# Kernel tuning notes

Hardware: AMD Instinct MI355X
Metric: run time of the kernel (lower is better)

Reference implementation:

```python
import jax, jax.numpy as jnp
import numpy as np

D_MODEL = 64

def setup_inputs() -> dict:
    key = jax.random.key(0)
    k1, k2, k3, k4 = jax.random.split(key, 4)
    B, T, E = 4, 4096, 128
    x = jax.random.normal(k1, (B, T, E), dtype=jnp.float32)
    # nn.Linear weights, stored transposed as (in, out) for x @ W
    s = 1.0 / np.sqrt(E)
    Wq = jax.random.uniform(k2, (E, D_MODEL), jnp.float32, -s, s)
    Wk = jax.random.uniform(k3, (E, D_MODEL), jnp.float32, -s, s)
    Wv = jax.random.uniform(k4, (E, D_MODEL), jnp.float32, -s, s)
    return {"x": x, "Wq": Wq, "Wk": Wk, "Wv": Wv}

def reference(x, Wq, Wk, Wv):
    B, T, E = x.shape
    q = jnp.einsum('bte,ed->btd', x, Wq)
    k = jnp.einsum('bte,ed->btd', x, Wk)
    v = jnp.einsum('bte,ed->btd', x, Wv)
    scores = jnp.einsum('bqd,bkd->bqk', q, k) / np.sqrt(D_MODEL)  # [B,T,T]
    causal = jnp.tril(jnp.ones((T, T), dtype=bool))
    scores = jnp.where(causal, scores, jnp.float32(-1e9))
    attn = jax.nn.softmax(scores, axis=-1)
    # dropout p=0.0 -> identity (eval-mode faithful)
    return jnp.einsum('bqk,bkd->bqd', attn, v)
```

## Files before the change

### kernel.cpp

```cpp
#include <hip/hip_runtime.h>
#include <hip/hip_bf16.h>


typedef __attribute__((ext_vector_type(4))) float  f32x4;
typedef __attribute__((ext_vector_type(4))) unsigned int u32x4;
typedef __attribute__((ext_vector_type(8))) __bf16 bf16x8;
typedef __attribute__((ext_vector_type(8))) unsigned short u16x8;
typedef __attribute__((ext_vector_type(4))) unsigned short u16x4;

#define T_SEQ 4096
#define DH    64
#define EDIM  128
#define KVB   64
#define QSCALE 0.18033688f
#define NTRI  528

__device__ __forceinline__ unsigned short f2bf(float f) {
    unsigned int x = __builtin_bit_cast(unsigned int, f);
    unsigned int r = x + 0x7fffu + ((x >> 16) & 1u);
    return (unsigned short)(r >> 16);
}

__device__ __forceinline__ unsigned int cvt_pk_bf16(float lo, float hi) {
    unsigned int d;
    asm("v_cvt_pk_bf16_f32 %0, %1, %2" : "=v"(d) : "v"(lo), "v"(hi));
    return d;
}

__device__ __forceinline__ f32x4 mfma_bf16(u16x8 a, u16x8 b, f32x4 c) {
    return __builtin_amdgcn_mfma_f32_16x16x32_bf16(
        __builtin_bit_cast(bf16x8, a), __builtin_bit_cast(bf16x8, b), c, 0, 0, 0);
}

__device__ __forceinline__ int kswz(int row, int bcol) {
    return row * 128 + (bcol ^ ((row & 7) << 4));
}
__device__ __forceinline__ int vswz(int row, int bcol) {
    return row * 256 + (bcol ^ ((row & 15) << 4));
}

__global__ __launch_bounds__(256) void prep_w_kernel(
    const float* __restrict__ wq, const float* __restrict__ wk,
    const float* __restrict__ wv, unsigned short* __restrict__ wt)
{
    int o = blockIdx.x * 256 + threadIdx.x;
    int m   = o >> 13;
    int rem = o & 8191;
    int d = rem >> 7, e = rem & 127;
    const float* W = (m == 0) ? wq : (m == 1) ? wk : wv;
    wt[o] = f2bf(W[e * DH + d]);
}

__global__ __launch_bounds__(64) void proj_kernel(
    const float* __restrict__ x, const unsigned short* __restrict__ wt,
    unsigned short* __restrict__ qw, unsigned short* __restrict__ kw,
    unsigned short* __restrict__ vt)
{
    const int l   = threadIdx.x;
    const int l15 = l & 15;
    const int lg  = l >> 4;
    const int row0 = blockIdx.x * 16;
    const int b    = row0 >> 12;
    const int t0   = row0 & 4095;

    u16x8 af[4];
    #pragma unroll
    for (int kt = 0; kt < 4; ++kt) {
        const float* xp = x + (row0 + l15) * EDIM + kt * 32 + lg * 8;
        f32x4 a = *(const f32x4*)xp;
        f32x4 bb = *(const f32x4*)(xp + 4);
        af[kt] = u16x8{ f2bf(a[0]), f2bf(a[1]), f2bf(a[2]), f2bf(a[3]),
                        f2bf(bb[0]), f2bf(bb[1]), f2bf(bb[2]), f2bf(bb[3]) };
    }

    unsigned short* outs[2] = { qw, kw };
    #pragma unroll
    for (int m = 0; m < 2; ++m) {
        #pragma unroll
        for (int nt = 0; nt < 4; ++nt) {
            f32x4 acc = {};
            #pragma unroll
            for (int kt = 0; kt < 4; ++kt) {
                u16x8 bfrag = *(const u16x8*)(wt + (m * 64 + nt * 16 + l15) * EDIM
                                                 + kt * 32 + lg * 8);
                acc = mfma_bf16(af[kt], bfrag, acc);
            }
            const float sc = (m == 0) ? QSCALE : 1.0f;
            #pragma unroll
            for (int r = 0; r < 4; ++r)
                outs[m][(row0 + lg * 4 + r) * DH + nt * 16 + l15] = f2bf(acc[r] * sc);
        }
    }

    #pragma unroll
    for (int nt = 0; nt < 4; ++nt) {
        f32x4 acc = {};
        #pragma unroll
        for (int kt = 0; kt < 4; ++kt) {
            u16x8 bfrag = *(const u16x8*)(wt + (2 * 64 + nt * 16 + l15) * EDIM
                                             + kt * 32 + lg * 8);
            acc = mfma_bf16(af[kt], bfrag, acc);
        }
        u16x4 pv = { f2bf(acc[0]), f2bf(acc[1]), f2bf(acc[2]), f2bf(acc[3]) };
        *(u16x4*)(vt + ((size_t)(b * DH + nt * 16 + l15)) * T_SEQ + t0 + lg * 4) = pv;
    }
}

__global__ __launch_bounds__(256, 4) void attn_partial_kernel(
    const unsigned short* __restrict__ qg, const unsigned short* __restrict__ kg,
    const unsigned short* __restrict__ vt,
    unsigned short* __restrict__ po, float* __restrict__ pm, float* __restrict__ pl)
{
    const int bid = blockIdx.x;
    const int b   = bid / NTRI;
    const int i   = bid - b * NTRI;
    int q = (int)((__builtin_sqrtf((float)(8 * i + 1)) - 1.0f) * 0.5f);
    while (q * (q + 1) / 2 > i) --q;
    while ((q + 1) * (q + 2) / 2 <= i) ++q;
    const int q128 = q;
    const int ch   = i - q * (q + 1) / 2;

    __shared__ char K_ldsb[128 * 128];
    __shared__ char V_ldsb[64 * 256];

    const int tid = threadIdx.x;
    const int w   = tid >> 6;
    const int l   = tid & 63;
    const int l15 = l & 15;
    const int lg  = l >> 4;

    const int base   = b * T_SEQ;
    const int qrow0w = q128 * 128 + w * 32;
    const int kvb    = ch * 128;

    const unsigned short* kgB = kg + (size_t)base * DH;
    const unsigned short* vtB = vt + (size_t)b * DH * T_SEQ;

    {
        u16x8 kr[4], vr[4];
        #pragma unroll
        for (int j = 0; j < 4; ++j) {
            int gi = tid + j * 256;
            kr[j] = *(const u16x8*)(kgB + (size_t)(kvb + (gi >> 3)) * DH + (gi & 7) * 8);
            vr[j] = *(const u16x8*)(vtB + (size_t)(gi >> 4) * T_SEQ + kvb + (gi & 15) * 8);
        }
        #pragma unroll
        for (int j = 0; j < 4; ++j) {
            int gi = tid + j * 256;
            *(u16x8*)&K_ldsb[kswz(gi >> 3, (gi & 7) * 16)]  = kr[j];
            *(u16x8*)&V_ldsb[vswz(gi >> 4, (gi & 15) * 16)] = vr[j];
        }
    }

    u16x8 qf[2][2];
    #pragma unroll
    for (int rt = 0; rt < 2; ++rt) {
        const unsigned short* qrow = qg + (base + qrow0w + rt * 16 + l15) * DH;
        qf[rt][0] = *(const u16x8*)(qrow + 0 + lg * 8);
        qf[rt][1] = *(const u16x8*)(qrow + 32 + lg * 8);
    }

    f32x4 o_acc[2][4];
    float m_run[2], l_run[2];
    #pragma unroll
    for (int rt = 0; rt < 2; ++rt) {
        #pragma unroll
        for (int dt = 0; dt < 4; ++dt) o_acc[rt][dt] = f32x4{};
        m_run[rt] = -1e30f; l_run[rt] = 0.0f;
    }

    const int src0 = l15 + 32 * (lg & 1);
    const int src1 = src0 + 16;
    const bool hi  = (lg >> 1) != 0;

    __syncthreads();

    #pragma unroll
    for (int tt = 0; tt < 2; ++tt) {
        const int kv0 = kvb + tt * 64;
        if (kv0 > qrow0w + 31) continue;

        u16x8 kf[4][2];
        #pragma unroll
        for (int nt = 0; nt < 4; ++nt)
            #pragma unroll
            for (int kt = 0; kt < 2; ++kt) {
                int krow = tt * 64 + nt * 16 + l15;
                kf[nt][kt] = *(const u16x8*)&K_ldsb[kswz(krow, kt * 64 + lg * 16)];
            }

        f32x4 s[2][4];
        __builtin_amdgcn_s_setprio(1);
        #pragma unroll
        for (int rt = 0; rt < 2; ++rt)
            #pragma unroll
            for (int nt = 0; nt < 4; ++nt) {
                f32x4 a = {};
                a = mfma_bf16(kf[nt][0], qf[rt][0], a);
                a = mfma_bf16(kf[nt][1], qf[rt][1], a);
                s[rt][nt] = a;
            }
        __builtin_amdgcn_s_setprio(0);

        if (kv0 + KVB - 1 > qrow0w) {
            #pragma unroll
            for (int rt = 0; rt < 2; ++rt)
                #pragma unroll
                for (int nt = 0; nt < 4; ++nt)
                    #pragma unroll
                    for (int rr = 0; rr < 4; ++rr) {
                        int kj = kv0 + nt * 16 + lg * 4 + rr;
                        int qi = qrow0w + rt * 16 + l15;
                        if (kj > qi) s[rt][nt][rr] = -1e30f;
                    }
        }

        float sc2[2];
        bool grow = false;
        unsigned int pk[2][4][2];
        #pragma unroll
        for (int rt = 0; rt < 2; ++rt) {
            float mx = s[rt][0][0];
            #pragma unroll
            for (int nt = 0; nt < 4; ++nt)
                #pragma unroll
                for (int rr = 0; rr < 4; ++rr)
                    mx = fmaxf(mx, s[rt][nt][rr]);
            mx = fmaxf(mx, __shfl_xor(mx, 16));
            mx = fmaxf(mx, __shfl_xor(mx, 32));

            float mold = m_run[rt];
            float mnew = fmaxf(mold, mx);
            grow |= (mx > mold);
            float sc = exp2f(mold - mnew);
            sc2[rt] = sc;
            m_run[rt] = mnew;

            float rs = 0.0f;
            #pragma unroll
            for (int nt = 0; nt < 4; ++nt)
                #pragma unroll
                for (int rr = 0; rr < 4; ++rr) {
                    float p = exp2f(s[rt][nt][rr] - mnew);
                    s[rt][nt][rr] = p;
                    rs += p;
                }
            rs += __shfl_xor(rs, 16);
            rs += __shfl_xor(rs, 32);
            l_run[rt] = l_run[rt] * sc + rs;

            #pragma unroll
            for (int nt = 0; nt < 4; ++nt) {
                pk[rt][nt][0] = cvt_pk_bf16(s[rt][nt][0], s[rt][nt][1]);
                pk[rt][nt][1] = cvt_pk_bf16(s[rt][nt][2], s[rt][nt][3]);
            }
        }
        if (__any(grow)) {
            #pragma unroll
            for (int rt = 0; rt < 2; ++rt)
                #pragma unroll
                for (int dt = 0; dt < 4; ++dt)
                    o_acc[rt][dt] *= sc2[rt];
        }

        __builtin_amdgcn_s_setprio(1);
        #pragma unroll
        for (int kt = 0; kt < 2; ++kt) {
            u16x8 vf[4];
            #pragma unroll
            for (int dt = 0; dt < 4; ++dt) {
                int vrow = dt * 16 + l15;
                vf[dt] = *(const u16x8*)&V_ldsb[vswz(vrow, tt * 128 + kt * 64 + lg * 16)];
            }
            #pragma unroll
            for (int rt = 0; rt < 2; ++rt) {
                unsigned int pb[4];
                #pragma unroll
                for (int t = 0; t < 4; ++t) {
                    int src = (t < 2) ? src0 : src1;
                    unsigned int pa  = __shfl(pk[rt][2 * kt][t & 1], src);
                    unsigned int pbv = __shfl(pk[rt][2 * kt + 1][t & 1], src);
                    pb[t] = hi ? pbv : pa;
                }
                u32x4 pbq = { pb[0], pb[1], pb[2], pb[3] };
                u16x8 pbf = __builtin_bit_cast(u16x8, pbq);
                #pragma unroll
                for (int dt = 0; dt < 4; ++dt)
                    o_acc[rt][dt] = mfma_bf16(vf[dt], pbf, o_acc[rt][dt]);
            }
        }
        __builtin_amdgcn_s_setprio(0);
    }

    const int pidx = bid;
    unsigned short* pob = po + (size_t)pidx * 8192;
    #pragma unroll
    for (int rt = 0; rt < 2; ++rt) {
        int row = w * 32 + rt * 16 + l15;
        #pragma unroll
        for (int dt = 0; dt < 4; ++dt) {
            unsigned int w0 = cvt_pk_bf16(o_acc[rt][dt][0], o_acc[rt][dt][1]);
            unsigned int w1 = cvt_pk_bf16(o_acc[rt][dt][2], o_acc[rt][dt][3]);
            *(unsigned int*)&pob[row * 64 + dt * 16 + lg * 4]     = w0;
            *(unsigned int*)&pob[row * 64 + dt * 16 + lg * 4 + 2] = w1;
        }
        if (lg == 0) {
            pm[pidx * 128 + row] = m_run[rt];
            pl[pidx * 128 + row] = l_run[rt];
        }
    }
}

__global__ __launch_bounds__(256) void attn_combine_kernel(
    const unsigned short* __restrict__ po, const float* __restrict__ pm,
    const float* __restrict__ pl, float* __restrict__ out)
{
    const int blk   = blockIdx.x;
    const int slice = blk & 3;
    const int tb    = blk >> 2;
    const int q128  = tb & 31;
    const int b     = tb >> 5;
    const int nch   = q128 + 1;
    const int bslot = b * NTRI + q128 * (q128 + 1) / 2;
    const int row   = slice * 32 + (threadIdx.x >> 3);
    const int d0    = (threadIdx.x & 7) * 8;

    float m_i[32];
    #pragma unroll
    for (int i = 0; i < 32; ++i) {
        int ii = (i < nch) ? i : 0;
        m_i[i] = pm[(bslot + ii) * 128 + row];
    }
    float mstar = m_i[0];
    #pragma unroll
    for (int i = 1; i < 32; ++i)
        if (i < nch) mstar = fmaxf(mstar, m_i[i]);

    float lsum = 0.0f;
    float a[8] = {};
    #pragma unroll
    for (int i = 0; i < 32; ++i) {
        if (i < nch) {
            float wi = exp2f(m_i[i] - mstar);
            lsum += wi * pl[(bslot + i) * 128 + row];
            u16x8 v = *(const u16x8*)&po[(size_t)(bslot + i) * 8192 + row * 64 + d0];
            #pragma unroll
            for (int j = 0; j < 8; ++j) {
                unsigned int u = (unsigned int)v[j] << 16;
                a[j] += wi * __builtin_bit_cast(float, u);
            }
        }
    }
    const float inv = 1.0f / lsum;
    float* op = out + (size_t)(b * T_SEQ + q128 * 128 + row) * DH + d0;
    f32x4 o0 = { a[0] * inv, a[1] * inv, a[2] * inv, a[3] * inv };
    f32x4 o1 = { a[4] * inv, a[5] * inv, a[6] * inv, a[7] * inv };
    *(f32x4*)op = o0;
    *(f32x4*)(op + 4) = o1;
}

__global__ __launch_bounds__(64, 4) void attn_direct_kernel(
    const unsigned short* __restrict__ qg, const unsigned short* __restrict__ kg,
    const unsigned short* __restrict__ vt, float* __restrict__ out)
{
    const int bid = blockIdx.x;
    const int q32 = bid & 127;
    const int b   = bid >> 7;
    const int l = threadIdx.x, l15 = l & 15, lg = l >> 4;
    const int qrow0 = q32 * 32;
    const int base  = b * T_SEQ;
    const unsigned short* kp = kg + (size_t)base * DH;
    const unsigned short* vp = vt + (size_t)b * DH * T_SEQ;

    u16x8 qf[2][2];
    #pragma unroll
    for (int rt = 0; rt < 2; ++rt) {
        const unsigned short* qrow = qg + (base + qrow0 + rt * 16 + l15) * DH;
        qf[rt][0] = *(const u16x8*)(qrow + 0 + lg * 8);
        qf[rt][1] = *(const u16x8*)(qrow + 32 + lg * 8);
    }

    f32x4 o_acc[2][4];
    float m_run[2], l_run[2];
    #pragma unroll
    for (int rt = 0; rt < 2; ++rt) {
        #pragma unroll
        for (int dt = 0; dt < 4; ++dt) o_acc[rt][dt] = f32x4{};
        m_run[rt] = -1e30f; l_run[rt] = 0.0f;
    }

    const int src0 = l15 + 32 * (lg & 1);
    const int src1 = src0 + 16;
    const bool hi  = (lg >> 1) != 0;

    for (int kv0 = 0; kv0 <= qrow0 + 31; kv0 += KVB) {
        u16x8 kf[4][2];
        #pragma unroll
        for (int nt = 0; nt < 4; ++nt)
            #pragma unroll
            for (int kt = 0; kt < 2; ++kt)
                kf[nt][kt] = *(const u16x8*)(kp + (kv0 + nt * 16 + l15) * DH
                                                + kt * 32 + lg * 8);
        f32x4 s[2][4];
        #pragma unroll
        for (int rt = 0; rt < 2; ++rt)
            #pragma unroll
            for (int nt = 0; nt < 4; ++nt) {
                f32x4 a = {};
                a = mfma_bf16(kf[nt][0], qf[rt][0], a);
                a = mfma_bf16(kf[nt][1], qf[rt][1], a);
                s[rt][nt] = a;
            }
        if (kv0 + KVB - 1 > qrow0) {
            #pragma unroll
            for (int rt = 0; rt < 2; ++rt)
                #pragma unroll
                for (int nt = 0; nt < 4; ++nt)
                    #pragma unroll
                    for (int rr = 0; rr < 4; ++rr) {
                        int kj = kv0 + nt * 16 + lg * 4 + rr;
                        int qi = qrow0 + rt * 16 + l15;
                        if (kj > qi) s[rt][nt][rr] = -1e30f;
                    }
        }
        float sc2[2];
        bool grow = false;
        unsigned int pk[2][4][2];
        #pragma unroll
        for (int rt = 0; rt < 2; ++rt) {
            float mx = s[rt][0][0];
            #pragma unroll
            for (int nt = 0; nt < 4; ++nt)
                #pragma unroll
                for (int rr = 0; rr < 4; ++rr)
                    mx = fmaxf(mx, s[rt][nt][rr]);
            mx = fmaxf(mx, __shfl_xor(mx, 16));
            mx = fmaxf(mx, __shfl_xor(mx, 32));
            float mold = m_run[rt];
            float mnew = fmaxf(mold, mx);
            grow |= (mx > mold);
            float sc = exp2f(mold - mnew);
            sc2[rt] = sc;
            m_run[rt] = mnew;
            float rs = 0.0f;
            #pragma unroll
            for (int nt = 0; nt < 4; ++nt)
                #pragma unroll
                for (int rr = 0; rr < 4; ++rr) {
                    float p = exp2f(s[rt][nt][rr] - mnew);
                    s[rt][nt][rr] = p;
                    rs += p;
                }
            rs += __shfl_xor(rs, 16);
            rs += __shfl_xor(rs, 32);
            l_run[rt] = l_run[rt] * sc + rs;
            #pragma unroll
            for (int nt = 0; nt < 4; ++nt) {
                pk[rt][nt][0] = cvt_pk_bf16(s[rt][nt][0], s[rt][nt][1]);
                pk[rt][nt][1] = cvt_pk_bf16(s[rt][nt][2], s[rt][nt][3]);
            }
        }
        if (__any(grow)) {
            #pragma unroll
            for (int rt = 0; rt < 2; ++rt)
                #pragma unroll
                for (int dt = 0; dt < 4; ++dt)
                    o_acc[rt][dt] *= sc2[rt];
        }
        #pragma unroll
        for (int kt = 0; kt < 2; ++kt) {
            u16x8 vf[4];
            #pragma unroll
            for (int dt = 0; dt < 4; ++dt)
                vf[dt] = *(const u16x8*)(vp + (size_t)(dt * 16 + l15) * T_SEQ
                                            + kv0 + kt * 32 + lg * 8);
            #pragma unroll
            for (int rt = 0; rt < 2; ++rt) {
                unsigned int pb[4];
                #pragma unroll
                for (int t = 0; t < 4; ++t) {
                    int src = (t < 2) ? src0 : src1;
                    unsigned int pa  = __shfl(pk[rt][2 * kt][t & 1], src);
                    unsigned int pbv = __shfl(pk[rt][2 * kt + 1][t & 1], src);
                    pb[t] = hi ? pbv : pa;
                }
                u32x4 pbq = { pb[0], pb[1], pb[2], pb[3] };
                u16x8 pbf = __builtin_bit_cast(u16x8, pbq);
                #pragma unroll
                for (int dt = 0; dt < 4; ++dt)
                    o_acc[rt][dt] = mfma_bf16(vf[dt], pbf, o_acc[rt][dt]);
            }
        }
    }

    #pragma unroll
    for (int rt = 0; rt < 2; ++rt) {
        float inv = 1.0f / l_run[rt];
        int row = base + qrow0 + rt * 16 + l15;
        #pragma unroll
        for (int dt = 0; dt < 4; ++dt) {
            f32x4 ov = o_acc[rt][dt] * inv;
            *(f32x4*)&out[(size_t)row * DH + dt * 16 + lg * 4] = ov;
        }
    }
}

extern "C" void kernel_launch(void* const* d_in, const int* in_sizes, int n_in,
                              void* d_out, int out_size, void* d_ws, size_t ws_size,
                              hipStream_t stream)
{
    const float* x  = (const float*)d_in[0];
    const float* wq = (const float*)d_in[1];
    const float* wk = (const float*)d_in[2];
    const float* wv = (const float*)d_in[3];
    float* out = (float*)d_out;

    unsigned short* wt = (unsigned short*)d_ws;
    unsigned short* qw = (unsigned short*)((char*)d_ws + 65536);
    unsigned short* kw = qw + (size_t)16384 * DH;
    unsigned short* vt = kw + (size_t)16384 * DH;

    const size_t slots  = 4u * NTRI;
    const size_t po_off = 65536u + 3u * 16384u * DH * 2u;
    const size_t po_sz  = slots * 8192 * 2;
    const size_t pm_off = po_off + po_sz;
    const size_t pl_off = pm_off + slots * 128 * 4;
    const size_t need   = pl_off + slots * 128 * 4;

    prep_w_kernel<<<96, 256, 0, stream>>>(wq, wk, wv, wt);
    proj_kernel<<<1024, 64, 0, stream>>>(x, wt, qw, kw, vt);

    if (ws_size >= need) {
        unsigned short* po = (unsigned short*)((char*)d_ws + po_off);
        float* pm = (float*)((char*)d_ws + pm_off);
        float* pl = (float*)((char*)d_ws + pl_off);
        attn_partial_kernel<<<4 * NTRI, 256, 0, stream>>>(qw, kw, vt, po, pm, pl);
        attn_combine_kernel<<<4 * 32 * 4, 256, 0, stream>>>(po, pm, pl, out);
    } else {
        attn_direct_kernel<<<4 * 128, 64, 0, stream>>>(qw, kw, vt, out);
    }
}
```

Baseline: 60.02 us.

## Process two KV chunks per attention block with register prefetch

Each partial-attention block now covers up to 256 keys instead of 128, which cuts the number of blocks from 528 to 272 per batch and halves the partial outputs the combine kernel reads. The second 128-key chunk is loaded into registers while the first is computed, then written to LDS between barriers. The row-sum shuffles are moved out of the inner loop to a single reduction at the end, and the max and sum reductions use a tree order. The trade-offs are fewer blocks to fill the GPU, longer serial work per block, and extra barriers.

```diff
diff --git a/kernel.cpp b/kernel.cpp
--- a/kernel.cpp
+++ b/kernel.cpp
@@ -13,7 +13,7 @@
 #define EDIM  128
 #define KVB   64
 #define QSCALE 0.18033688f
-#define NTRI  528
+#define NPAIR 272
 
 __device__ __forceinline__ unsigned short f2bf(float f) {
     unsigned int x = __builtin_bit_cast(unsigned int, f);
@@ -106,19 +106,42 @@
     }
 }
 
+__device__ __forceinline__ void loadKV(u16x8 kr[4], u16x8 vr[4],
+                                       const unsigned short* kgB,
+                                       const unsigned short* vtB,
+                                       int kv0, int tid) {
+    #pragma unroll
+    for (int j = 0; j < 4; ++j) {
+        int gi = tid + j * 256;
+        kr[j] = *(const u16x8*)(kgB + (size_t)(kv0 + (gi >> 3)) * DH + (gi & 7) * 8);
+        vr[j] = *(const u16x8*)(vtB + (size_t)(gi >> 4) * T_SEQ + kv0 + (gi & 15) * 8);
+    }
+}
+__device__ __forceinline__ void writeKV(const u16x8 kr[4], const u16x8 vr[4],
+                                        char* K_ldsb, char* V_ldsb, int tid) {
+    #pragma unroll
+    for (int j = 0; j < 4; ++j) {
+        int gi = tid + j * 256;
+        *(u16x8*)&K_ldsb[kswz(gi >> 3, (gi & 7) * 16)]  = kr[j];
+        *(u16x8*)&V_ldsb[vswz(gi >> 4, (gi & 15) * 16)] = vr[j];
+    }
+}
+
 __global__ __launch_bounds__(256, 4) void attn_partial_kernel(
     const unsigned short* __restrict__ qg, const unsigned short* __restrict__ kg,
     const unsigned short* __restrict__ vt,
     unsigned short* __restrict__ po, float* __restrict__ pm, float* __restrict__ pl)
 {
     const int bid = blockIdx.x;
-    const int b   = bid / NTRI;
-    const int i   = bid - b * NTRI;
-    int q = (int)((__builtin_sqrtf((float)(8 * i + 1)) - 1.0f) * 0.5f);
-    while (q * (q + 1) / 2 > i) --q;
-    while ((q + 1) * (q + 2) / 2 <= i) ++q;
-    const int q128 = q;
-    const int ch   = i - q * (q + 1) / 2;
+    const int b   = bid / NPAIR;
+    const int i   = bid - b * NPAIR;
+    int k = (int)((__builtin_sqrtf((float)(4 * i + 1)) - 1.0f) * 0.5f);
+    while (k * (k + 1) > i) --k;
+    while ((k + 1) * (k + 2) <= i) ++k;
+    const int r    = i - k * (k + 1);
+    const int hiq  = (r >= k + 1);
+    const int q128 = 2 * k + hiq;
+    const int ch   = hiq ? r - (k + 1) : r;
 
     __shared__ char K_ldsb[128 * 128];
     __shared__ char V_ldsb[64 * 256];
@@ -131,26 +154,12 @@
 
     const int base   = b * T_SEQ;
     const int qrow0w = q128 * 128 + w * 32;
-    const int kvb    = ch * 128;
+    const int kvb    = ch * 256;
+    const int kve    = min(kvb + 256, q128 * 128 + 128);
+    const bool ng2   = (kve - kvb) > 128;
 
     const unsigned short* kgB = kg + (size_t)base * DH;
     const unsigned short* vtB = vt + (size_t)b * DH * T_SEQ;
-
-    {
-        u16x8 kr[4], vr[4];
-        #pragma unroll
-        for (int j = 0; j < 4; ++j) {
-            int gi = tid + j * 256;
-            kr[j] = *(const u16x8*)(kgB + (size_t)(kvb + (gi >> 3)) * DH + (gi & 7) * 8);
-            vr[j] = *(const u16x8*)(vtB + (size_t)(gi >> 4) * T_SEQ + kvb + (gi & 15) * 8);
-        }
-        #pragma unroll
-        for (int j = 0; j < 4; ++j) {
-            int gi = tid + j * 256;
-            *(u16x8*)&K_ldsb[kswz(gi >> 3, (gi & 7) * 16)]  = kr[j];
-            *(u16x8*)&V_ldsb[vswz(gi >> 4, (gi & 15) * 16)] = vr[j];
-        }
-    }
 
     u16x8 qf[2][2];
     #pragma unroll
@@ -173,12 +182,8 @@
     const int src1 = src0 + 16;
     const bool hi  = (lg >> 1) != 0;
 
-    __syncthreads();
-
-    #pragma unroll
-    for (int tt = 0; tt < 2; ++tt) {
-        const int kv0 = kvb + tt * 64;
-        if (kv0 > qrow0w + 31) continue;
+    auto compute_tile = [&](int kv0, int tt) {
+        if (kv0 > qrow0w + 31) return;
 
         u16x8 kf[4][2];
         #pragma unroll
@@ -220,12 +225,15 @@
         unsigned int pk[2][4][2];
         #pragma unroll
         for (int rt = 0; rt < 2; ++rt) {
-            float mx = s[rt][0][0];
-            #pragma unroll
-            for (int nt = 0; nt < 4; ++nt)
-                #pragma unroll
-                for (int rr = 0; rr < 4; ++rr)
-                    mx = fmaxf(mx, s[rt][nt][rr]);
+            float t0 = fmaxf(fmaxf(s[rt][0][0], s[rt][0][1]),
+                             fmaxf(s[rt][0][2], s[rt][0][3]));
+            float t1 = fmaxf(fmaxf(s[rt][1][0], s[rt][1][1]),
+                             fmaxf(s[rt][1][2], s[rt][1][3]));
+            float t2 = fmaxf(fmaxf(s[rt][2][0], s[rt][2][1]),
+                             fmaxf(s[rt][2][2], s[rt][2][3]));
+            float t3 = fmaxf(fmaxf(s[rt][3][0], s[rt][3][1]),
+                             fmaxf(s[rt][3][2], s[rt][3][3]));
+            float mx = fmaxf(fmaxf(t0, t1), fmaxf(t2, t3));
             mx = fmaxf(mx, __shfl_xor(mx, 16));
             mx = fmaxf(mx, __shfl_xor(mx, 32));
 
@@ -236,23 +244,22 @@
             sc2[rt] = sc;
             m_run[rt] = mnew;
 
-            float rs = 0.0f;
+            float e[4][4];
             #pragma unroll
             for (int nt = 0; nt < 4; ++nt)
                 #pragma unroll
-                for (int rr = 0; rr < 4; ++rr) {
-                    float p = exp2f(s[rt][nt][rr] - mnew);
-                    s[rt][nt][rr] = p;
-                    rs += p;
-                }
-            rs += __shfl_xor(rs, 16);
-            rs += __shfl_xor(rs, 32);
-            l_run[rt] = l_run[rt] * sc + rs;
+                for (int rr = 0; rr < 4; ++rr)
+                    e[nt][rr] = exp2f(s[rt][nt][rr] - mnew);
+            float s0 = (e[0][0] + e[0][1]) + (e[0][2] + e[0][3]);
+            float s1 = (e[1][0] + e[1][1]) + (e[1][2] + e[1][3]);
+            float s2 = (e[2][0] + e[2][1]) + (e[2][2] + e[2][3]);
+            float s3 = (e[3][0] + e[3][1]) + (e[3][2] + e[3][3]);
+            l_run[rt] = l_run[rt] * sc + ((s0 + s1) + (s2 + s3));
 
             #pragma unroll
             for (int nt = 0; nt < 4; ++nt) {
-                pk[rt][nt][0] = cvt_pk_bf16(s[rt][nt][0], s[rt][nt][1]);
-                pk[rt][nt][1] = cvt_pk_bf16(s[rt][nt][2], s[rt][nt][3]);
+                pk[rt][nt][0] = cvt_pk_bf16(e[nt][0], e[nt][1]);
+                pk[rt][nt][1] = cvt_pk_bf16(e[nt][2], e[nt][3]);
             }
         }
         if (__any(grow)) {
@@ -290,12 +297,32 @@
             }
         }
         __builtin_amdgcn_s_setprio(0);
+    };
+
+    u16x8 kr[4], vr[4];
+    loadKV(kr, vr, kgB, vtB, kvb, tid);
+    writeKV(kr, vr, K_ldsb, V_ldsb, tid);
+    __syncthreads();
+
+    if (ng2) loadKV(kr, vr, kgB, vtB, kvb + 128, tid);
+    compute_tile(kvb, 0);
+    compute_tile(kvb + 64, 1);
+
+    if (ng2) {
+        __syncthreads();
+        writeKV(kr, vr, K_ldsb, V_ldsb, tid);
+        __syncthreads();
+        compute_tile(kvb + 128, 0);
+        compute_tile(kvb + 192, 1);
     }
 
     const int pidx = bid;
     unsigned short* pob = po + (size_t)pidx * 8192;
     #pragma unroll
     for (int rt = 0; rt < 2; ++rt) {
+        float lt = l_run[rt];
+        lt += __shfl_xor(lt, 16);
+        lt += __shfl_xor(lt, 32);
         int row = w * 32 + rt * 16 + l15;
         #pragma unroll
         for (int dt = 0; dt < 4; ++dt) {
@@ -306,7 +333,7 @@
         }
         if (lg == 0) {
             pm[pidx * 128 + row] = m_run[rt];
-            pl[pidx * 128 + row] = l_run[rt];
+            pl[pidx * 128 + row] = lt;
         }
     }
 }
@@ -320,26 +347,27 @@
     const int tb    = blk >> 2;
     const int q128  = tb & 31;
     const int b     = tb >> 5;
-    const int nch   = q128 + 1;
-    const int bslot = b * NTRI + q128 * (q128 + 1) / 2;
+    const int kk    = q128 >> 1;
+    const int nch   = kk + 1;
+    const int bslot = b * NPAIR + kk * (kk + 1) + (q128 & 1) * (kk + 1);
     const int row   = slice * 32 + (threadIdx.x >> 3);
     const int d0    = (threadIdx.x & 7) * 8;
 
-    float m_i[32];
-    #pragma unroll
-    for (int i = 0; i < 32; ++i) {
+    float m_i[16];
+    #pragma unroll
+    for (int i = 0; i < 16; ++i) {
         int ii = (i < nch) ? i : 0;
         m_i[i] = pm[(bslot + ii) * 128 + row];
     }
     float mstar = m_i[0];
     #pragma unroll
-    for (int i = 1; i < 32; ++i)
+    for (int i = 1; i < 16; ++i)
         if (i < nch) mstar = fmaxf(mstar, m_i[i]);
 
     float lsum = 0.0f;
     float a[8] = {};
     #pragma unroll
-    for (int i = 0; i < 32; ++i) {
+    for (int i = 0; i < 16; ++i) {
         if (i < nch) {
             float wi = exp2f(m_i[i] - mstar);
             lsum += wi * pl[(bslot + i) * 128 + row];
@@ -520,7 +548,7 @@
     unsigned short* kw = qw + (size_t)16384 * DH;
     unsigned short* vt = kw + (size_t)16384 * DH;
 
-    const size_t slots  = 4u * NTRI;
+    const size_t slots  = 4u * NPAIR;
     const size_t po_off = 65536u + 3u * 16384u * DH * 2u;
     const size_t po_sz  = slots * 8192 * 2;
     const size_t pm_off = po_off + po_sz;
@@ -534,7 +562,7 @@
         unsigned short* po = (unsigned short*)((char*)d_ws + po_off);
         float* pm = (float*)((char*)d_ws + pm_off);
         float* pl = (float*)((char*)d_ws + pl_off);
-        attn_partial_kernel<<<4 * NTRI, 256, 0, stream>>>(qw, kw, vt, po, pm, pl);
+        attn_partial_kernel<<<4 * NPAIR, 256, 0, stream>>>(qw, kw, vt, po, pm, pl);
         attn_combine_kernel<<<4 * 32 * 4, 256, 0, stream>>>(po, pm, pl, out);
     } else {
         attn_direct_kernel<<<4 * 128, 64, 0, stream>>>(qw, kw, vt, out);
```

After: 65.92 us. 9.8% more time.

## Widen split-KV attention blocks to 256 query rows with XCD-aware block mapping

Applied to the files above, without the earlier changes.

Each partial-attention block now handles 256 query rows (8 waves, 512 threads) against one 128-key chunk, so each K/V chunk loaded into LDS is reused by twice as many queries and the block count roughly halves. Block indices are remapped so that consecutive tiles are spread across the 8 XCDs. The triangular index decoding, the partial buffer strides and the combine kernel's slot indexing are updated to match. The cost is more chunks on the diagonal where half the rows are fully masked, which adds wasted work, plus higher register and occupancy pressure at 512 threads per block.

```diff
diff --git a/kernel.cpp b/kernel.cpp
--- a/kernel.cpp
+++ b/kernel.cpp
@@ -13,7 +13,7 @@
 #define EDIM  128
 #define KVB   64
 #define QSCALE 0.18033688f
-#define NTRI  528
+#define NTRI2 272
 
 __device__ __forceinline__ unsigned short f2bf(float f) {
     unsigned int x = __builtin_bit_cast(unsigned int, f);
@@ -106,19 +106,19 @@
     }
 }
 
-__global__ __launch_bounds__(256, 4) void attn_partial_kernel(
+__global__ __launch_bounds__(512, 6) void attn_partial_kernel(
     const unsigned short* __restrict__ qg, const unsigned short* __restrict__ kg,
     const unsigned short* __restrict__ vt,
     unsigned short* __restrict__ po, float* __restrict__ pm, float* __restrict__ pl)
 {
-    const int bid = blockIdx.x;
-    const int b   = bid / NTRI;
-    const int i   = bid - b * NTRI;
-    int q = (int)((__builtin_sqrtf((float)(8 * i + 1)) - 1.0f) * 0.5f);
-    while (q * (q + 1) / 2 > i) --q;
-    while ((q + 1) * (q + 2) / 2 <= i) ++q;
-    const int q128 = q;
-    const int ch   = i - q * (q + 1) / 2;
+    const int phys = blockIdx.x;
+    const int bid  = (phys & 7) * 136 + (phys >> 3);
+    const int b    = bid / NTRI2;
+    const int i    = bid - b * NTRI2;
+    int Q = (int)((__builtin_sqrtf((float)(4 * i + 1)) - 1.0f) * 0.5f);
+    while (Q * (Q + 1) > i) --Q;
+    while ((Q + 1) * (Q + 2) <= i) ++Q;
+    const int ch = i - Q * (Q + 1);
 
     __shared__ char K_ldsb[128 * 128];
     __shared__ char V_ldsb[64 * 256];
@@ -130,23 +130,23 @@
     const int lg  = l >> 4;
 
     const int base   = b * T_SEQ;
-    const int qrow0w = q128 * 128 + w * 32;
+    const int qrow0w = Q * 256 + w * 32;
     const int kvb    = ch * 128;
 
     const unsigned short* kgB = kg + (size_t)base * DH;
     const unsigned short* vtB = vt + (size_t)b * DH * T_SEQ;
 
     {
-        u16x8 kr[4], vr[4];
-        #pragma unroll
-        for (int j = 0; j < 4; ++j) {
-            int gi = tid + j * 256;
+        u16x8 kr[2], vr[2];
+        #pragma unroll
+        for (int j = 0; j < 2; ++j) {
+            int gi = tid + j * 512;
             kr[j] = *(const u16x8*)(kgB + (size_t)(kvb + (gi >> 3)) * DH + (gi & 7) * 8);
             vr[j] = *(const u16x8*)(vtB + (size_t)(gi >> 4) * T_SEQ + kvb + (gi & 15) * 8);
         }
         #pragma unroll
-        for (int j = 0; j < 4; ++j) {
-            int gi = tid + j * 256;
+        for (int j = 0; j < 2; ++j) {
+            int gi = tid + j * 512;
             *(u16x8*)&K_ldsb[kswz(gi >> 3, (gi & 7) * 16)]  = kr[j];
             *(u16x8*)&V_ldsb[vswz(gi >> 4, (gi & 15) * 16)] = vr[j];
         }
@@ -293,7 +293,7 @@
     }
 
     const int pidx = bid;
-    unsigned short* pob = po + (size_t)pidx * 8192;
+    unsigned short* pob = po + (size_t)pidx * 16384;
     #pragma unroll
     for (int rt = 0; rt < 2; ++rt) {
         int row = w * 32 + rt * 16 + l15;
@@ -305,8 +305,8 @@
             *(unsigned int*)&pob[row * 64 + dt * 16 + lg * 4 + 2] = w1;
         }
         if (lg == 0) {
-            pm[pidx * 128 + row] = m_run[rt];
-            pl[pidx * 128 + row] = l_run[rt];
+            pm[pidx * 256 + row] = m_run[rt];
+            pl[pidx * 256 + row] = l_run[rt];
         }
     }
 }
@@ -320,16 +320,18 @@
     const int tb    = blk >> 2;
     const int q128  = tb & 31;
     const int b     = tb >> 5;
-    const int nch   = q128 + 1;
-    const int bslot = b * NTRI + q128 * (q128 + 1) / 2;
-    const int row   = slice * 32 + (threadIdx.x >> 3);
+    const int Q     = q128 >> 1;
+    const int h     = q128 & 1;
+    const int nch   = 2 * Q + 2;
+    const int bslot = b * NTRI2 + Q * (Q + 1);
+    const int rsl   = h * 128 + slice * 32 + (threadIdx.x >> 3);
     const int d0    = (threadIdx.x & 7) * 8;
 
     float m_i[32];
     #pragma unroll
     for (int i = 0; i < 32; ++i) {
         int ii = (i < nch) ? i : 0;
-        m_i[i] = pm[(bslot + ii) * 128 + row];
+        m_i[i] = pm[(bslot + ii) * 256 + rsl];
     }
     float mstar = m_i[0];
     #pragma unroll
@@ -342,8 +344,8 @@
     for (int i = 0; i < 32; ++i) {
         if (i < nch) {
             float wi = exp2f(m_i[i] - mstar);
-            lsum += wi * pl[(bslot + i) * 128 + row];
-            u16x8 v = *(const u16x8*)&po[(size_t)(bslot + i) * 8192 + row * 64 + d0];
+            lsum += wi * pl[(bslot + i) * 256 + rsl];
+            u16x8 v = *(const u16x8*)&po[(size_t)(bslot + i) * 16384 + rsl * 64 + d0];
             #pragma unroll
             for (int j = 0; j < 8; ++j) {
                 unsigned int u = (unsigned int)v[j] << 16;
@@ -352,7 +354,7 @@
         }
     }
     const float inv = 1.0f / lsum;
-    float* op = out + (size_t)(b * T_SEQ + q128 * 128 + row) * DH + d0;
+    float* op = out + (size_t)(b * T_SEQ + q128 * 128 + slice * 32 + (threadIdx.x >> 3)) * DH + d0;
     f32x4 o0 = { a[0] * inv, a[1] * inv, a[2] * inv, a[3] * inv };
     f32x4 o1 = { a[4] * inv, a[5] * inv, a[6] * inv, a[7] * inv };
     *(f32x4*)op = o0;
@@ -520,12 +522,12 @@
     unsigned short* kw = qw + (size_t)16384 * DH;
     unsigned short* vt = kw + (size_t)16384 * DH;
 
-    const size_t slots  = 4u * NTRI;
+    const size_t slots  = 4u * NTRI2;
     const size_t po_off = 65536u + 3u * 16384u * DH * 2u;
-    const size_t po_sz  = slots * 8192 * 2;
+    const size_t po_sz  = slots * 16384 * 2;
     const size_t pm_off = po_off + po_sz;
-    const size_t pl_off = pm_off + slots * 128 * 4;
-    const size_t need   = pl_off + slots * 128 * 4;
+    const size_t pl_off = pm_off + slots * 256 * 4;
+    const size_t need   = pl_off + slots * 256 * 4;
 
     prep_w_kernel<<<96, 256, 0, stream>>>(wq, wk, wv, wt);
     proj_kernel<<<1024, 64, 0, stream>>>(x, wt, qw, kw, vt);
@@ -534,7 +536,7 @@
         unsigned short* po = (unsigned short*)((char*)d_ws + po_off);
         float* pm = (float*)((char*)d_ws + pm_off);
         float* pl = (float*)((char*)d_ws + pl_off);
-        attn_partial_kernel<<<4 * NTRI, 256, 0, stream>>>(qw, kw, vt, po, pm, pl);
+        attn_partial_kernel<<<4 * NTRI2, 512, 0, stream>>>(qw, kw, vt, po, pm, pl);
         attn_combine_kernel<<<4 * 32 * 4, 256, 0, stream>>>(po, pm, pl, out);
     } else {
         attn_direct_kernel<<<4 * 128, 64, 0, stream>>>(qw, kw, vt, out);
```

Result: slower. 97.30 us (+62.1%).
